# Kernel optimization log

Hardware: AMD Instinct MI355X
Metric: run time of the kernel (lower is better)

## Reference

```python
import jax, jax.numpy as jnp
import numpy as np

B, T, IN, H, L, OUT = 32, 512, 256, 1024, 2, 256


def setup_inputs() -> dict:
    key = jax.random.key(0)
    ks = jax.random.split(key, 12)
    s_in = 1.0 / np.sqrt(H)
    inp = {
        "input": jax.random.normal(ks[0], (B, T, IN), dtype=jnp.float32),
        # layer 0 GRU params (PyTorch layout: [3H, in], gate order r,z,n)
        "w_ih0": jax.random.uniform(ks[1], (3 * H, IN), jnp.float32, -s_in, s_in),
        "w_hh0": jax.random.uniform(ks[2], (3 * H, H), jnp.float32, -s_in, s_in),
        "b_ih0": jax.random.uniform(ks[3], (3 * H,), jnp.float32, -s_in, s_in),
        "b_hh0": jax.random.uniform(ks[4], (3 * H,), jnp.float32, -s_in, s_in),
        # layer 1 GRU params
        "w_ih1": jax.random.uniform(ks[5], (3 * H, H), jnp.float32, -s_in, s_in),
        "w_hh1": jax.random.uniform(ks[6], (3 * H, H), jnp.float32, -s_in, s_in),
        "b_ih1": jax.random.uniform(ks[7], (3 * H,), jnp.float32, -s_in, s_in),
        "b_hh1": jax.random.uniform(ks[8], (3 * H,), jnp.float32, -s_in, s_in),
        # final linear
        "fc_w": jax.random.uniform(ks[9], (OUT, H), jnp.float32, -s_in, s_in),
        "fc_b": jax.random.uniform(ks[10], (OUT,), jnp.float32, -s_in, s_in),
    }
    return inp


def _gru_layer(x, h0, w_ih, w_hh, b_ih, b_hh):
    # x: [B, T, D]; h0: [B, H]. Precompute all input projections at once.
    gx = jnp.einsum("btd,gd->btg", x, w_ih) + b_ih  # [B, T, 3H]

    def step(h, gx_t):
        gh = h @ w_hh.T + b_hh  # [B, 3H]
        xr, xz, xn = jnp.split(gx_t, 3, axis=-1)
        hr, hz, hn = jnp.split(gh, 3, axis=-1)
        r = jax.nn.sigmoid(xr + hr)
        z = jax.nn.sigmoid(xz + hz)
        n = jnp.tanh(xn + r * hn)
        h_new = (1.0 - z) * n + z * h
        return h_new, h_new

    h_last, hs = jax.lax.scan(step, h0, jnp.swapaxes(gx, 0, 1))  # hs: [T, B, H]
    return jnp.swapaxes(hs, 0, 1), h_last


def reference(input, w_ih0, w_hh0, b_ih0, b_hh0, w_ih1, w_hh1, b_ih1, b_hh1, fc_w, fc_b):
    b = input.shape[0]
    h0 = jnp.zeros((b, H), dtype=input.dtype)
    out0, h_last0 = _gru_layer(input, h0, w_ih0, w_hh0, b_ih0, b_hh0)
    out1, h_last1 = _gru_layer(out0, h0, w_ih1, w_hh1, b_ih1, b_hh1)
    h_n = jnp.stack([h_last0, h_last1], axis=0)  # [L, B, H]
    logits = out1[:, -1, :] @ fc_w.T + fc_b  # [B, OUT]
    return jax.nn.sigmoid(logits), h_n
```

## Files before the change

kernel.cpp:

```cpp
#include <hip/hip_runtime.h>

#define BB 32
#define TT 512
#define INW 256
#define HH 1024
#define OUTW 256
#define SLOT 32768

typedef __attribute__((ext_vector_type(8))) short short8;
typedef __attribute__((ext_vector_type(4))) float floatx4;
typedef __attribute__((ext_vector_type(4))) unsigned int uint4v;

#define SENT 0x7F807F80u

#define RSWZ(i) ((i) ^ ((((i) >> 5) & 3) << 2))

__device__ __forceinline__ unsigned short f2bf(float f) {
    unsigned int u = __float_as_uint(f);
    u = (u + 0x7fffu + ((u >> 16) & 1u)) >> 16;
    return (unsigned short)u;
}
__device__ __forceinline__ float bf2f(unsigned short h) {
    return __uint_as_float(((unsigned int)h) << 16);
}
__device__ __forceinline__ float fast_tanh(float x) {
    return 2.f / (1.f + __expf(-2.f * x)) - 1.f;
}
__device__ __forceinline__ float tree8(const float* p) {
    return ((p[0] + p[1]) + (p[2] + p[3])) + ((p[4] + p[5]) + (p[6] + p[7]));
}

__global__ void cast_f32_bf16(const float* __restrict__ src,
                              unsigned short* __restrict__ dst, int n) {
    int i = blockIdx.x * blockDim.x + threadIdx.x;
    int stride = gridDim.x * blockDim.x;
    for (; i < n; i += stride) dst[i] = f2bf(src[i]);
}

__global__ void fill_sent(uint4v* __restrict__ dst, size_t n4) {
    size_t i = (size_t)blockIdx.x * blockDim.x + threadIdx.x;
    size_t stride = (size_t)gridDim.x * blockDim.x;
    uint4v v = {SENT, SENT, SENT, SENT};
    for (; i < n4; i += stride) dst[i] = v;
}

template <int K>
__global__ __launch_bounds__(256) void gemm_gx(const unsigned short* __restrict__ X,
                                               const unsigned short* __restrict__ W,
                                               const float* __restrict__ bias,
                                               unsigned short* __restrict__ Cout) {
    __shared__ __align__(16) unsigned short As[64 * 40];
    __shared__ __align__(16) unsigned short Bs[64 * 40];
    int bid = blockIdx.x;
    int tn = bid % 48, tm = bid / 48;
    int tid = threadIdx.x;
    int lane = tid & 63, wv = tid >> 6;
    int wm = wv >> 1, wn = wv & 1;
    int l15 = lane & 15, q = lane >> 4;
    floatx4 acc[2][2] = {};
    int r = tid >> 2, kq = (tid & 3) * 8;
    const unsigned short* xrow = X + (size_t)(tm * 64 + r) * K;
    const unsigned short* wrow = W + (size_t)(tn * 64 + r) * K;
    const int NK = K / 32;
    for (int kk = 0; kk < NK; ++kk) {
        int k0 = kk * 32;
        *(short8*)&As[r * 40 + kq] = *(const short8*)&xrow[k0 + kq];
        *(short8*)&Bs[r * 40 + kq] = *(const short8*)&wrow[k0 + kq];
        __syncthreads();
        short8 a0 = *(const short8*)&As[(wm * 32 + l15) * 40 + q * 8];
        short8 a1 = *(const short8*)&As[(wm * 32 + 16 + l15) * 40 + q * 8];
        short8 b0 = *(const short8*)&Bs[(wn * 32 + l15) * 40 + q * 8];
        short8 b1 = *(const short8*)&Bs[(wn * 32 + 16 + l15) * 40 + q * 8];
        acc[0][0] = __builtin_amdgcn_mfma_f32_16x16x32_bf16(a0, b0, acc[0][0], 0, 0, 0);
        acc[0][1] = __builtin_amdgcn_mfma_f32_16x16x32_bf16(a0, b1, acc[0][1], 0, 0, 0);
        acc[1][0] = __builtin_amdgcn_mfma_f32_16x16x32_bf16(a1, b0, acc[1][0], 0, 0, 0);
        acc[1][1] = __builtin_amdgcn_mfma_f32_16x16x32_bf16(a1, b1, acc[1][1], 0, 0, 0);
        __syncthreads();
    }
    for (int mi = 0; mi < 2; ++mi)
        for (int ni = 0; ni < 2; ++ni) {
            int col = tn * 64 + wn * 32 + ni * 16 + l15;
            float bv = bias[col];
            int row0 = tm * 64 + wm * 32 + mi * 16 + q * 4;
            for (int rr = 0; rr < 4; ++rr) {
                Cout[(size_t)(row0 + rr) * 3072 + col] = f2bf(acc[mi][ni][rr] + bv);
            }
        }
}

__global__ __launch_bounds__(512, 2) void gru_fused(
    const unsigned short* __restrict__ gx0, const unsigned short* __restrict__ whh0,
    const float* __restrict__ bhh0, const unsigned short* __restrict__ wih1,
    const unsigned short* __restrict__ whh1, const float* __restrict__ bih1,
    const float* __restrict__ bhh1, unsigned short* __restrict__ ring0,
    unsigned short* __restrict__ ring1, float* __restrict__ hn0,
    float* __restrict__ hn1, unsigned int* __restrict__ flags) {
    __shared__ __align__(16) float red[8 * 6 * 64 * 4];
    const int bid = blockIdx.x;
    const int tid = threadIdx.x;
    const int lane = tid & 63, wv = tid >> 6;
    const int l15 = lane & 15, q = lane >> 4;
    const int gb = tid >> 3, gjh = tid & 7;
    const int gmi = gb >> 4, greg = gb & 3;
    const int grl = ((gb & 15) >> 2) * 16 + 2 * gjh;

    if (bid < 64) {
        const int j0 = bid * 16;
        const int kbase = wv * 128;
        const unsigned int* fl0 = flags + ((bid & 7) << 8);
        short8 Wr[4], Wz[4], Wn[4];
        {
            const unsigned short* wr0 = whh0 + (size_t)(j0 + l15) * HH;
            const unsigned short* wr1 = whh0 + (size_t)(1024 + j0 + l15) * HH;
            const unsigned short* wr2 = whh0 + (size_t)(2048 + j0 + l15) * HH;
#pragma unroll
            for (int s = 0; s < 4; ++s) {
                int k = kbase + s * 32 + q * 8;
                Wr[s] = *(const short8*)&wr0[k];
                Wz[s] = *(const short8*)&wr1[k];
                Wn[s] = *(const short8*)&wr2[k];
            }
        }
        float bR[2], bZ[2], bN[2], hpriv[2] = {0.f, 0.f};
        unsigned int pxr = 0, pxz = 0, pxn = 0;
        const unsigned short* gxp = nullptr;
        if (tid < 256) {
            int jj = j0 + 2 * gjh;
#pragma unroll
            for (int i = 0; i < 2; ++i) {
                bR[i] = bhh0[jj + i];
                bZ[i] = bhh0[1024 + jj + i];
                bN[i] = bhh0[2048 + jj + i];
            }
            gxp = gx0 + (size_t)gb * TT * 3072 + jj;
            pxr = *(const unsigned int*)(gxp);
            pxz = *(const unsigned int*)(gxp + 1024);
            pxn = *(const unsigned int*)(gxp + 2048);
        }

        for (int t = 0; t < TT; ++t) {
            if (t > 0 && wv == 0) {
                unsigned int target = (unsigned int)t;
                while (true) {
                    unsigned int v = __hip_atomic_load(fl0 + lane, __ATOMIC_RELAXED,
                                                       __HIP_MEMORY_SCOPE_AGENT);
                    if (__all((int)(v >= target))) break;
                }
            }
            __syncthreads();
            const unsigned short* hc = ring0 + (size_t)t * SLOT;
            unsigned int cxr = pxr, cxz = pxz, cxn = pxn;

            const unsigned short* ap[4];
#pragma unroll
            for (int s = 0; s < 4; ++s) {
                int k = kbase + s * 32 + q * 8;
                ap[s] = hc + ((k >> 4) << 9) + (l15 << 4) + (k & 15);
            }
            uint4v r0[4], r1[4];
            while (true) {
#pragma unroll
                for (int s = 0; s < 4; ++s) {
                    asm volatile("global_load_dwordx4 %0, %1, off sc0 sc1"
                                 : "=&v"(r0[s]) : "v"(ap[s]));
                    asm volatile("global_load_dwordx4 %0, %1, off offset:512 sc0 sc1"
                                 : "=&v"(r1[s]) : "v"(ap[s]));
                }
                asm volatile("s_waitcnt vmcnt(0)"
                             : "+v"(r0[0]), "+v"(r0[1]), "+v"(r0[2]), "+v"(r0[3]),
                               "+v"(r1[0]), "+v"(r1[1]), "+v"(r1[2]), "+v"(r1[3])
                             :: "memory");
                unsigned bad = 0;
#pragma unroll
                for (int s = 0; s < 4; ++s) {
                    bad |= (unsigned)(r0[s][0] == SENT) | (unsigned)(r0[s][1] == SENT) |
                           (unsigned)(r0[s][2] == SENT) | (unsigned)(r0[s][3] == SENT);
                    bad |= (unsigned)(r1[s][0] == SENT) | (unsigned)(r1[s][1] == SENT) |
                           (unsigned)(r1[s][2] == SENT) | (unsigned)(r1[s][3] == SENT);
                }
                if (!__any((int)bad)) break;
            }

            floatx4 acc[6] = {};
#pragma unroll
            for (int s = 0; s < 4; ++s) {
                short8 a0 = __builtin_bit_cast(short8, r0[s]);
                short8 a1 = __builtin_bit_cast(short8, r1[s]);
                acc[0] = __builtin_amdgcn_mfma_f32_16x16x32_bf16(a0, Wr[s], acc[0], 0, 0, 0);
                acc[1] = __builtin_amdgcn_mfma_f32_16x16x32_bf16(a0, Wz[s], acc[1], 0, 0, 0);
                acc[2] = __builtin_amdgcn_mfma_f32_16x16x32_bf16(a0, Wn[s], acc[2], 0, 0, 0);
                acc[3] = __builtin_amdgcn_mfma_f32_16x16x32_bf16(a1, Wr[s], acc[3], 0, 0, 0);
                acc[4] = __builtin_amdgcn_mfma_f32_16x16x32_bf16(a1, Wz[s], acc[4], 0, 0, 0);
                acc[5] = __builtin_amdgcn_mfma_f32_16x16x32_bf16(a1, Wn[s], acc[5], 0, 0, 0);
            }
#pragma unroll
            for (int tl = 0; tl < 6; ++tl)
                *(floatx4*)&red[RSWZ(((wv * 6 + tl) * 64 + lane) * 4)] = acc[tl];
            __syncthreads();

            float hnew[2];
            if (tid < 256) {
#pragma unroll
                for (int i = 0; i < 2; ++i) {
                    int rl = grl + i;
                    float pr[8], pz[8], pn[8];
#pragma unroll
                    for (int w = 0; w < 8; ++w) {
                        pr[w] = red[RSWZ(((w * 6 + gmi * 3 + 0) * 64 + rl) * 4 + greg)];
                        pz[w] = red[RSWZ(((w * 6 + gmi * 3 + 1) * 64 + rl) * 4 + greg)];
                        pn[w] = red[RSWZ(((w * 6 + gmi * 3 + 2) * 64 + rl) * 4 + greg)];
                    }
                    float gr = tree8(pr), gz = tree8(pz), gn = tree8(pn);
                    float xr = bf2f((unsigned short)(i ? (cxr >> 16) : (cxr & 0xffffu)));
                    float xz = bf2f((unsigned short)(i ? (cxz >> 16) : (cxz & 0xffffu)));
                    float xn = bf2f((unsigned short)(i ? (cxn >> 16) : (cxn & 0xffffu)));
                    float rg = 1.f / (1.f + __expf(-(xr + gr + bR[i])));
                    float zg = 1.f / (1.f + __expf(-(xz + gz + bZ[i])));
                    float ng = fast_tanh(xn + rg * (gn + bN[i]));
                    hnew[i] = (1.f - zg) * ng + zg * hpriv[i];
                    hpriv[i] = hnew[i];
                }
                unsigned int hpack =
                    (unsigned int)f2bf(hnew[0]) | ((unsigned int)f2bf(hnew[1]) << 16);
                unsigned int* dst =
                    (unsigned int*)(ring0 + (size_t)(t + 1) * SLOT) + (bid << 8) + tid;
                __hip_atomic_store(dst, hpack, __ATOMIC_RELAXED,
                                   __HIP_MEMORY_SCOPE_AGENT);
            }
            __syncthreads();
            if (tid < 8)
                __hip_atomic_store(flags + (tid << 8) + bid, (unsigned int)(t + 1),
                                   __ATOMIC_RELAXED, __HIP_MEMORY_SCOPE_AGENT);
            if (tid < 256) {
                if (t == TT - 1) {
                    hn0[gb * HH + j0 + 2 * gjh] = hnew[0];
                    hn0[gb * HH + j0 + 2 * gjh + 1] = hnew[1];
                }
                if (t + 1 < TT) {
                    const unsigned short* g2 = gxp + (size_t)(t + 1) * 3072;
                    pxr = *(const unsigned int*)(g2);
                    pxz = *(const unsigned int*)(g2 + 1024);
                    pxn = *(const unsigned int*)(g2 + 2048);
                }
            }
        }
    } else {
        const int b2 = bid - 64;
        const int j0 = b2 * 16;
        const bool isx = (wv >= 4);
        const int kbase = (wv & 3) * 256;
        const unsigned int* fl1 = flags + 2048 + ((b2 & 7) << 8);
        const unsigned int* fl0 = flags + ((b2 & 7) << 8);
        short8 Wr[8], Wz[8], Wn[8];
        {
            const unsigned short* wsrc = isx ? wih1 : whh1;
            const unsigned short* w0 = wsrc + (size_t)(j0 + l15) * HH;
            const unsigned short* w1 = wsrc + (size_t)(1024 + j0 + l15) * HH;
            const unsigned short* w2 = wsrc + (size_t)(2048 + j0 + l15) * HH;
#pragma unroll
            for (int s = 0; s < 8; ++s) {
                int k = kbase + s * 32 + q * 8;
                Wr[s] = *(const short8*)&w0[k];
                Wz[s] = *(const short8*)&w1[k];
                Wn[s] = *(const short8*)&w2[k];
            }
        }
        float cR[2], cZ[2], cNx[2], cNh[2], hpriv[2] = {0.f, 0.f};
        if (tid < 256) {
            int jj = j0 + 2 * gjh;
#pragma unroll
            for (int i = 0; i < 2; ++i) {
                cR[i] = bih1[jj + i] + bhh1[jj + i];
                cZ[i] = bih1[1024 + jj + i] + bhh1[1024 + jj + i];
                cNx[i] = bih1[2048 + jj + i];
                cNh[i] = bhh1[2048 + jj + i];
            }
        }

        for (int t = 0; t < TT; ++t) {
            if (t > 0 && wv == 0) {
                unsigned int target = (unsigned int)t;
                while (true) {
                    unsigned int v = __hip_atomic_load(fl1 + lane, __ATOMIC_RELAXED,
                                                       __HIP_MEMORY_SCOPE_AGENT);
                    if (__all((int)(v >= target))) break;
                }
            }
            if (wv == 4) {
                unsigned int target = (unsigned int)(t + 1);
                while (true) {
                    unsigned int v = __hip_atomic_load(fl0 + lane, __ATOMIC_RELAXED,
                                                       __HIP_MEMORY_SCOPE_AGENT);
                    if (__all((int)(v >= target))) break;
                }
            }
            __syncthreads();
            const unsigned short* src =
                isx ? (ring0 + (size_t)(t + 1) * SLOT) : (ring1 + (size_t)t * SLOT);

            const unsigned short* ap[8];
#pragma unroll
            for (int s = 0; s < 8; ++s) {
                int k = kbase + s * 32 + q * 8;
                ap[s] = src + ((k >> 4) << 9) + (l15 << 4) + (k & 15);
            }
            uint4v r0[8], r1[8];
            while (true) {
#pragma unroll
                for (int s = 0; s < 8; ++s) {
                    asm volatile("global_load_dwordx4 %0, %1, off sc0 sc1"
                                 : "=&v"(r0[s]) : "v"(ap[s]));
                    asm volatile("global_load_dwordx4 %0, %1, off offset:512 sc0 sc1"
                                 : "=&v"(r1[s]) : "v"(ap[s]));
                }
                asm volatile("s_waitcnt vmcnt(0)"
                             : "+v"(r0[0]), "+v"(r0[1]), "+v"(r0[2]), "+v"(r0[3]),
                               "+v"(r0[4]), "+v"(r0[5]), "+v"(r0[6]), "+v"(r0[7]),
                               "+v"(r1[0]), "+v"(r1[1]), "+v"(r1[2]), "+v"(r1[3]),
                               "+v"(r1[4]), "+v"(r1[5]), "+v"(r1[6]), "+v"(r1[7])
                             :: "memory");
                unsigned bad = 0;
#pragma unroll
                for (int s = 0; s < 8; ++s) {
                    bad |= (unsigned)(r0[s][0] == SENT) | (unsigned)(r0[s][1] == SENT) |
                           (unsigned)(r0[s][2] == SENT) | (unsigned)(r0[s][3] == SENT);
                    bad |= (unsigned)(r1[s][0] == SENT) | (unsigned)(r1[s][1] == SENT) |
                           (unsigned)(r1[s][2] == SENT) | (unsigned)(r1[s][3] == SENT);
                }
                if (!__any((int)bad)) break;
            }

            floatx4 acc[6] = {};
#pragma unroll
            for (int s = 0; s < 8; ++s) {
                short8 a0 = __builtin_bit_cast(short8, r0[s]);
                short8 a1 = __builtin_bit_cast(short8, r1[s]);
                acc[0] = __builtin_amdgcn_mfma_f32_16x16x32_bf16(a0, Wr[s], acc[0], 0, 0, 0);
                acc[1] = __builtin_amdgcn_mfma_f32_16x16x32_bf16(a0, Wz[s], acc[1], 0, 0, 0);
                acc[2] = __builtin_amdgcn_mfma_f32_16x16x32_bf16(a0, Wn[s], acc[2], 0, 0, 0);
                acc[3] = __builtin_amdgcn_mfma_f32_16x16x32_bf16(a1, Wr[s], acc[3], 0, 0, 0);
                acc[4] = __builtin_amdgcn_mfma_f32_16x16x32_bf16(a1, Wz[s], acc[4], 0, 0, 0);
                acc[5] = __builtin_amdgcn_mfma_f32_16x16x32_bf16(a1, Wn[s], acc[5], 0, 0, 0);
            }
#pragma unroll
            for (int tl = 0; tl < 6; ++tl)
                *(floatx4*)&red[RSWZ(((wv * 6 + tl) * 64 + lane) * 4)] = acc[tl];
            __syncthreads();

            float hnew[2];
            if (tid < 256) {
#pragma unroll
                for (int i = 0; i < 2; ++i) {
                    int rl = grl + i;
                    float pr[8], pz[8], ph[4], px[4];
#pragma unroll
                    for (int w = 0; w < 8; ++w) {
                        pr[w] = red[RSWZ(((w * 6 + gmi * 3 + 0) * 64 + rl) * 4 + greg)];
                        pz[w] = red[RSWZ(((w * 6 + gmi * 3 + 1) * 64 + rl) * 4 + greg)];
                    }
#pragma unroll
                    for (int w = 0; w < 4; ++w)
                        ph[w] = red[RSWZ(((w * 6 + gmi * 3 + 2) * 64 + rl) * 4 + greg)];
#pragma unroll
                    for (int w = 4; w < 8; ++w)
                        px[w - 4] = red[RSWZ(((w * 6 + gmi * 3 + 2) * 64 + rl) * 4 + greg)];
                    float gr = tree8(pr), gz = tree8(pz);
                    float hn = (ph[0] + ph[1]) + (ph[2] + ph[3]);
                    float xn = (px[0] + px[1]) + (px[2] + px[3]);
                    float rg = 1.f / (1.f + __expf(-(gr + cR[i])));
                    float zg = 1.f / (1.f + __expf(-(gz + cZ[i])));
                    float ng = fast_tanh(xn + cNx[i] + rg * (hn + cNh[i]));
                    hnew[i] = (1.f - zg) * ng + zg * hpriv[i];
                    hpriv[i] = hnew[i];
                }
                unsigned int hpack =
                    (unsigned int)f2bf(hnew[0]) | ((unsigned int)f2bf(hnew[1]) << 16);
                unsigned int* dst =
                    (unsigned int*)(ring1 + (size_t)(t + 1) * SLOT) + (b2 << 8) + tid;
                __hip_atomic_store(dst, hpack, __ATOMIC_RELAXED,
                                   __HIP_MEMORY_SCOPE_AGENT);
            }
            __syncthreads();
            if (tid < 8)
                __hip_atomic_store(flags + 2048 + (tid << 8) + b2, (unsigned int)(t + 1),
                                   __ATOMIC_RELAXED, __HIP_MEMORY_SCOPE_AGENT);
            if (tid < 256 && t == TT - 1) {
                hn1[gb * HH + j0 + 2 * gjh] = hnew[0];
                hn1[gb * HH + j0 + 2 * gjh + 1] = hnew[1];
            }
        }
    }
}

__global__ void fc_out(const unsigned short* __restrict__ h1bf,
                       const float* __restrict__ fcw, const float* __restrict__ fcb,
                       float* __restrict__ out) {
    int b = blockIdx.x, o = threadIdx.x;
    const float* wr = fcw + (size_t)o * HH;
    float acc = fcb[o];
    for (int k = 0; k < HH; k += 16) {
        const unsigned short* hp = h1bf + ((k >> 4) << 9) + (b << 4);
#pragma unroll
        for (int i = 0; i < 16; ++i) acc += bf2f(hp[i]) * wr[k + i];
    }
    out[b * OUTW + o] = 1.f / (1.f + expf(-acc));
}

extern "C" void kernel_launch(void* const* d_in, const int* in_sizes, int n_in,
                              void* d_out, int out_size, void* d_ws, size_t ws_size,
                              hipStream_t stream) {
    (void)in_sizes; (void)n_in; (void)out_size; (void)ws_size;
    const float* input = (const float*)d_in[0];
    const float* w_ih0 = (const float*)d_in[1];
    const float* w_hh0 = (const float*)d_in[2];
    const float* b_ih0 = (const float*)d_in[3];
    const float* b_hh0 = (const float*)d_in[4];
    const float* w_ih1 = (const float*)d_in[5];
    const float* w_hh1 = (const float*)d_in[6];
    const float* b_ih1 = (const float*)d_in[7];
    const float* b_hh1 = (const float*)d_in[8];
    const float* fc_w = (const float*)d_in[9];
    const float* fc_b = (const float*)d_in[10];
    float* out = (float*)d_out;

    char* ws = (char*)d_ws;
    size_t off = 0;
    auto alloc = [&](size_t bytes) {
        void* p = ws + off;
        off += (bytes + 255) & ~(size_t)255;
        return p;
    };
    unsigned int* flags = (unsigned int*)alloc(16384);
    unsigned short* ring0 = (unsigned short*)alloc((size_t)(TT + 1) * SLOT * 2);
    unsigned short* ring1 = (unsigned short*)alloc((size_t)(TT + 1) * SLOT * 2);
    unsigned short* gx0 = (unsigned short*)alloc((size_t)16384 * 3072 * 2);
    unsigned short* in_bf = (unsigned short*)alloc((size_t)16384 * 256 * 2);
    unsigned short* wih0_bf = (unsigned short*)alloc((size_t)3072 * 256 * 2);
    unsigned short* whh0_bf = (unsigned short*)alloc((size_t)3072 * 1024 * 2);
    unsigned short* wih1_bf = (unsigned short*)alloc((size_t)3072 * 1024 * 2);
    unsigned short* whh1_bf = (unsigned short*)alloc((size_t)3072 * 1024 * 2);

    {
        size_t total_bytes = (size_t)2 * (TT + 1) * SLOT * 2;
        fill_sent<<<1024, 256, 0, stream>>>((uint4v*)ring0, total_bytes / 16);
    }

    cast_f32_bf16<<<256, 256, 0, stream>>>(input, in_bf, 16384 * 256);
    cast_f32_bf16<<<64, 256, 0, stream>>>(w_ih0, wih0_bf, 3072 * 256);
    cast_f32_bf16<<<256, 256, 0, stream>>>(w_hh0, whh0_bf, 3072 * 1024);
    cast_f32_bf16<<<256, 256, 0, stream>>>(w_ih1, wih1_bf, 3072 * 1024);
    cast_f32_bf16<<<256, 256, 0, stream>>>(w_hh1, whh1_bf, 3072 * 1024);

    hipMemsetAsync(flags, 0, 16384, stream);
    hipMemsetAsync(ring0, 0, (size_t)SLOT * 2, stream);
    hipMemsetAsync(ring1, 0, (size_t)SLOT * 2, stream);

    gemm_gx<256><<<12288, 256, 0, stream>>>(in_bf, wih0_bf, b_ih0, gx0);

    gru_fused<<<128, 512, 0, stream>>>(gx0, whh0_bf, b_hh0, wih1_bf, whh1_bf, b_ih1,
                                       b_hh1, ring0, ring1, out + 8192,
                                       out + 8192 + 32768, flags);

    fc_out<<<32, 256, 0, stream>>>(ring1 + (size_t)TT * SLOT, fc_w, fc_b, out);
}
```

Baseline: 2.455 ms.

## Drop flag barriers, rely on sentinel polling and split matmul/gate warps

Removes the per-step flag arrays and atomic flag polling, so consumers detect readiness only by spinning on sentinel values in the ring buffers. Layer 0 now uses four matmul warps over K=256 each and four dedicated gate warps, and the gate step for t-1 runs concurrently with the matmul for t, software-pipelining the recurrence. Layer 1 gate warps likewise compute the previous step's output before issuing their input-projection loads. This is meant to cut cross-block synchronisation latency per timestep, at the cost of heavier register use per warp (the occupancy hint is dropped) and reliance on sentinel-only visibility ordering.

```diff
diff --git a/kernel.cpp b/kernel.cpp
--- a/kernel.cpp
+++ b/kernel.cpp
@@ -88,43 +88,100 @@
         }
 }
 
-__global__ __launch_bounds__(512, 2) void gru_fused(
+__device__ __forceinline__ void spin_load8(const unsigned short* base, int kbase,
+                                           int l15, int q, uint4v r0[8],
+                                           uint4v r1[8]) {
+    const unsigned short* ap[8];
+#pragma unroll
+    for (int s = 0; s < 8; ++s) {
+        int k = kbase + s * 32 + q * 8;
+        ap[s] = base + ((k >> 4) << 9) + (l15 << 4) + (k & 15);
+    }
+    while (true) {
+#pragma unroll
+        for (int s = 0; s < 8; ++s) {
+            asm volatile("global_load_dwordx4 %0, %1, off sc0 sc1"
+                         : "=&v"(r0[s]) : "v"(ap[s]));
+            asm volatile("global_load_dwordx4 %0, %1, off offset:512 sc0 sc1"
+                         : "=&v"(r1[s]) : "v"(ap[s]));
+        }
+        asm volatile("s_waitcnt vmcnt(0)"
+                     : "+v"(r0[0]), "+v"(r0[1]), "+v"(r0[2]), "+v"(r0[3]),
+                       "+v"(r0[4]), "+v"(r0[5]), "+v"(r0[6]), "+v"(r0[7]),
+                       "+v"(r1[0]), "+v"(r1[1]), "+v"(r1[2]), "+v"(r1[3]),
+                       "+v"(r1[4]), "+v"(r1[5]), "+v"(r1[6]), "+v"(r1[7])
+                     :: "memory");
+        unsigned bad = 0;
+#pragma unroll
+        for (int s = 0; s < 8; ++s) {
+            bad |= (unsigned)(r0[s][0] == SENT) | (unsigned)(r0[s][1] == SENT) |
+                   (unsigned)(r0[s][2] == SENT) | (unsigned)(r0[s][3] == SENT);
+            bad |= (unsigned)(r1[s][0] == SENT) | (unsigned)(r1[s][1] == SENT) |
+                   (unsigned)(r1[s][2] == SENT) | (unsigned)(r1[s][3] == SENT);
+        }
+        if (!__any((int)bad)) break;
+    }
+}
+
+__device__ __forceinline__ void mfma8(const uint4v r0[8], const uint4v r1[8],
+                                      const short8 Wr[8], const short8 Wz[8],
+                                      const short8 Wn[8], floatx4 acc[6]) {
+#pragma unroll
+    for (int s = 0; s < 8; ++s) {
+        short8 a0 = __builtin_bit_cast(short8, r0[s]);
+        short8 a1 = __builtin_bit_cast(short8, r1[s]);
+        acc[0] = __builtin_amdgcn_mfma_f32_16x16x32_bf16(a0, Wr[s], acc[0], 0, 0, 0);
+        acc[1] = __builtin_amdgcn_mfma_f32_16x16x32_bf16(a0, Wz[s], acc[1], 0, 0, 0);
+        acc[2] = __builtin_amdgcn_mfma_f32_16x16x32_bf16(a0, Wn[s], acc[2], 0, 0, 0);
+        acc[3] = __builtin_amdgcn_mfma_f32_16x16x32_bf16(a1, Wr[s], acc[3], 0, 0, 0);
+        acc[4] = __builtin_amdgcn_mfma_f32_16x16x32_bf16(a1, Wz[s], acc[4], 0, 0, 0);
+        acc[5] = __builtin_amdgcn_mfma_f32_16x16x32_bf16(a1, Wn[s], acc[5], 0, 0, 0);
+    }
+}
+
+__device__ __forceinline__ void hoist_w(const unsigned short* wsrc, int j0, int l15,
+                                        int q, int kbase, short8 Wr[8], short8 Wz[8],
+                                        short8 Wn[8]) {
+    const unsigned short* w0 = wsrc + (size_t)(j0 + l15) * HH;
+    const unsigned short* w1 = wsrc + (size_t)(1024 + j0 + l15) * HH;
+    const unsigned short* w2 = wsrc + (size_t)(2048 + j0 + l15) * HH;
+#pragma unroll
+    for (int s = 0; s < 8; ++s) {
+        int k = kbase + s * 32 + q * 8;
+        Wr[s] = *(const short8*)&w0[k];
+        Wz[s] = *(const short8*)&w1[k];
+        Wn[s] = *(const short8*)&w2[k];
+    }
+}
+
+__global__ __launch_bounds__(512) void gru_fused(
     const unsigned short* __restrict__ gx0, const unsigned short* __restrict__ whh0,
     const float* __restrict__ bhh0, const unsigned short* __restrict__ wih1,
     const unsigned short* __restrict__ whh1, const float* __restrict__ bih1,
     const float* __restrict__ bhh1, unsigned short* __restrict__ ring0,
     unsigned short* __restrict__ ring1, float* __restrict__ hn0,
-    float* __restrict__ hn1, unsigned int* __restrict__ flags) {
+    float* __restrict__ hn1) {
     __shared__ __align__(16) float red[8 * 6 * 64 * 4];
     const int bid = blockIdx.x;
     const int tid = threadIdx.x;
     const int lane = tid & 63, wv = tid >> 6;
     const int l15 = lane & 15, q = lane >> 4;
-    const int gb = tid >> 3, gjh = tid & 7;
+    const bool isGate = (wv >= 4);
+    const int gtid = tid & 255;
+    const int gb = gtid >> 3, gjh = gtid & 7;
     const int gmi = gb >> 4, greg = gb & 3;
     const int grl = ((gb & 15) >> 2) * 16 + 2 * gjh;
 
     if (bid < 64) {
         const int j0 = bid * 16;
-        const int kbase = wv * 128;
-        const unsigned int* fl0 = flags + ((bid & 7) << 8);
-        short8 Wr[4], Wz[4], Wn[4];
-        {
-            const unsigned short* wr0 = whh0 + (size_t)(j0 + l15) * HH;
-            const unsigned short* wr1 = whh0 + (size_t)(1024 + j0 + l15) * HH;
-            const unsigned short* wr2 = whh0 + (size_t)(2048 + j0 + l15) * HH;
-#pragma unroll
-            for (int s = 0; s < 4; ++s) {
-                int k = kbase + s * 32 + q * 8;
-                Wr[s] = *(const short8*)&wr0[k];
-                Wz[s] = *(const short8*)&wr1[k];
-                Wn[s] = *(const short8*)&wr2[k];
-            }
-        }
+        const int kbase = (wv & 3) * 256;
+        short8 Wr[8], Wz[8], Wn[8];
+        if (!isGate) hoist_w(whh0, j0, l15, q, kbase, Wr, Wz, Wn);
+
         float bR[2], bZ[2], bN[2], hpriv[2] = {0.f, 0.f};
         unsigned int pxr = 0, pxz = 0, pxn = 0;
         const unsigned short* gxp = nullptr;
-        if (tid < 256) {
+        if (isGate) {
             int jj = j0 + 2 * gjh;
 #pragma unroll
             for (int i = 0; i < 2; ++i) {
@@ -138,79 +195,38 @@
             pxn = *(const unsigned int*)(gxp + 2048);
         }
 
-        for (int t = 0; t < TT; ++t) {
-            if (t > 0 && wv == 0) {
-                unsigned int target = (unsigned int)t;
-                while (true) {
-                    unsigned int v = __hip_atomic_load(fl0 + lane, __ATOMIC_RELAXED,
-                                                       __HIP_MEMORY_SCOPE_AGENT);
-                    if (__all((int)(v >= target))) break;
-                }
-            }
-            __syncthreads();
-            const unsigned short* hc = ring0 + (size_t)t * SLOT;
-            unsigned int cxr = pxr, cxz = pxz, cxn = pxn;
-
-            const unsigned short* ap[4];
-#pragma unroll
-            for (int s = 0; s < 4; ++s) {
-                int k = kbase + s * 32 + q * 8;
-                ap[s] = hc + ((k >> 4) << 9) + (l15 << 4) + (k & 15);
-            }
-            uint4v r0[4], r1[4];
-            while (true) {
-#pragma unroll
-                for (int s = 0; s < 4; ++s) {
-                    asm volatile("global_load_dwordx4 %0, %1, off sc0 sc1"
-                                 : "=&v"(r0[s]) : "v"(ap[s]));
-                    asm volatile("global_load_dwordx4 %0, %1, off offset:512 sc0 sc1"
-                                 : "=&v"(r1[s]) : "v"(ap[s]));
-                }
-                asm volatile("s_waitcnt vmcnt(0)"
-                             : "+v"(r0[0]), "+v"(r0[1]), "+v"(r0[2]), "+v"(r0[3]),
-                               "+v"(r1[0]), "+v"(r1[1]), "+v"(r1[2]), "+v"(r1[3])
-                             :: "memory");
-                unsigned bad = 0;
-#pragma unroll
-                for (int s = 0; s < 4; ++s) {
-                    bad |= (unsigned)(r0[s][0] == SENT) | (unsigned)(r0[s][1] == SENT) |
-                           (unsigned)(r0[s][2] == SENT) | (unsigned)(r0[s][3] == SENT);
-                    bad |= (unsigned)(r1[s][0] == SENT) | (unsigned)(r1[s][1] == SENT) |
-                           (unsigned)(r1[s][2] == SENT) | (unsigned)(r1[s][3] == SENT);
-                }
-                if (!__any((int)bad)) break;
-            }
-
+        for (int t = 0; t <= TT; ++t) {
             floatx4 acc[6] = {};
-#pragma unroll
-            for (int s = 0; s < 4; ++s) {
-                short8 a0 = __builtin_bit_cast(short8, r0[s]);
-                short8 a1 = __builtin_bit_cast(short8, r1[s]);
-                acc[0] = __builtin_amdgcn_mfma_f32_16x16x32_bf16(a0, Wr[s], acc[0], 0, 0, 0);
-                acc[1] = __builtin_amdgcn_mfma_f32_16x16x32_bf16(a0, Wz[s], acc[1], 0, 0, 0);
-                acc[2] = __builtin_amdgcn_mfma_f32_16x16x32_bf16(a0, Wn[s], acc[2], 0, 0, 0);
-                acc[3] = __builtin_amdgcn_mfma_f32_16x16x32_bf16(a1, Wr[s], acc[3], 0, 0, 0);
-                acc[4] = __builtin_amdgcn_mfma_f32_16x16x32_bf16(a1, Wz[s], acc[4], 0, 0, 0);
-                acc[5] = __builtin_amdgcn_mfma_f32_16x16x32_bf16(a1, Wn[s], acc[5], 0, 0, 0);
-            }
-#pragma unroll
-            for (int tl = 0; tl < 6; ++tl)
-                *(floatx4*)&red[RSWZ(((wv * 6 + tl) * 64 + lane) * 4)] = acc[tl];
-            __syncthreads();
-
-            float hnew[2];
-            if (tid < 256) {
+            bool doW = false;
+            if (!isGate) {
+                if (t < TT) {
+                    uint4v r0[8], r1[8];
+                    spin_load8(ring0 + (size_t)t * SLOT, kbase, l15, q, r0, r1);
+                    mfma8(r0, r1, Wr, Wz, Wn, acc);
+                    doW = true;
+                }
+            } else if (t > 0) {
+                unsigned int cxr = pxr, cxz = pxz, cxn = pxn;
+                if (t < TT) {
+                    const unsigned short* g2 = gxp + (size_t)t * 3072;
+                    pxr = *(const unsigned int*)(g2);
+                    pxz = *(const unsigned int*)(g2 + 1024);
+                    pxn = *(const unsigned int*)(g2 + 2048);
+                }
+                float hnew[2];
 #pragma unroll
                 for (int i = 0; i < 2; ++i) {
                     int rl = grl + i;
-                    float pr[8], pz[8], pn[8];
-#pragma unroll
-                    for (int w = 0; w < 8; ++w) {
+                    float pr[4], pz[4], pn[4];
+#pragma unroll
+                    for (int w = 0; w < 4; ++w) {
                         pr[w] = red[RSWZ(((w * 6 + gmi * 3 + 0) * 64 + rl) * 4 + greg)];
                         pz[w] = red[RSWZ(((w * 6 + gmi * 3 + 1) * 64 + rl) * 4 + greg)];
                         pn[w] = red[RSWZ(((w * 6 + gmi * 3 + 2) * 64 + rl) * 4 + greg)];
                     }
-                    float gr = tree8(pr), gz = tree8(pz), gn = tree8(pn);
+                    float gr = (pr[0] + pr[1]) + (pr[2] + pr[3]);
+                    float gz = (pz[0] + pz[1]) + (pz[2] + pz[3]);
+                    float gn = (pn[0] + pn[1]) + (pn[2] + pn[3]);
                     float xr = bf2f((unsigned short)(i ? (cxr >> 16) : (cxr & 0xffffu)));
                     float xz = bf2f((unsigned short)(i ? (cxz >> 16) : (cxz & 0xffffu)));
                     float xn = bf2f((unsigned short)(i ? (cxn >> 16) : (cxn & 0xffffu)));
@@ -223,50 +239,31 @@
                 unsigned int hpack =
                     (unsigned int)f2bf(hnew[0]) | ((unsigned int)f2bf(hnew[1]) << 16);
                 unsigned int* dst =
-                    (unsigned int*)(ring0 + (size_t)(t + 1) * SLOT) + (bid << 8) + tid;
+                    (unsigned int*)(ring0 + (size_t)t * SLOT) + (bid << 8) + gtid;
                 __hip_atomic_store(dst, hpack, __ATOMIC_RELAXED,
                                    __HIP_MEMORY_SCOPE_AGENT);
-            }
-            __syncthreads();
-            if (tid < 8)
-                __hip_atomic_store(flags + (tid << 8) + bid, (unsigned int)(t + 1),
-                                   __ATOMIC_RELAXED, __HIP_MEMORY_SCOPE_AGENT);
-            if (tid < 256) {
-                if (t == TT - 1) {
+                if (t == TT) {
                     hn0[gb * HH + j0 + 2 * gjh] = hnew[0];
                     hn0[gb * HH + j0 + 2 * gjh + 1] = hnew[1];
                 }
-                if (t + 1 < TT) {
-                    const unsigned short* g2 = gxp + (size_t)(t + 1) * 3072;
-                    pxr = *(const unsigned int*)(g2);
-                    pxz = *(const unsigned int*)(g2 + 1024);
-                    pxn = *(const unsigned int*)(g2 + 2048);
-                }
-            }
+            }
+            __syncthreads();
+            if (doW) {
+#pragma unroll
+                for (int tl = 0; tl < 6; ++tl)
+                    *(floatx4*)&red[RSWZ((((wv & 3) * 6 + tl) * 64 + lane) * 4)] = acc[tl];
+            }
+            __syncthreads();
         }
     } else {
         const int b2 = bid - 64;
         const int j0 = b2 * 16;
-        const bool isx = (wv >= 4);
         const int kbase = (wv & 3) * 256;
-        const unsigned int* fl1 = flags + 2048 + ((b2 & 7) << 8);
-        const unsigned int* fl0 = flags + ((b2 & 7) << 8);
         short8 Wr[8], Wz[8], Wn[8];
-        {
-            const unsigned short* wsrc = isx ? wih1 : whh1;
-            const unsigned short* w0 = wsrc + (size_t)(j0 + l15) * HH;
-            const unsigned short* w1 = wsrc + (size_t)(1024 + j0 + l15) * HH;
-            const unsigned short* w2 = wsrc + (size_t)(2048 + j0 + l15) * HH;
-#pragma unroll
-            for (int s = 0; s < 8; ++s) {
-                int k = kbase + s * 32 + q * 8;
-                Wr[s] = *(const short8*)&w0[k];
-                Wz[s] = *(const short8*)&w1[k];
-                Wn[s] = *(const short8*)&w2[k];
-            }
-        }
+        hoist_w(isGate ? wih1 : whh1, j0, l15, q, kbase, Wr, Wz, Wn);
+
         float cR[2], cZ[2], cNx[2], cNh[2], hpriv[2] = {0.f, 0.f};
-        if (tid < 256) {
+        if (isGate) {
             int jj = j0 + 2 * gjh;
 #pragma unroll
             for (int i = 0; i < 2; ++i) {
@@ -277,117 +274,68 @@
             }
         }
 
-        for (int t = 0; t < TT; ++t) {
-            if (t > 0 && wv == 0) {
-                unsigned int target = (unsigned int)t;
-                while (true) {
-                    unsigned int v = __hip_atomic_load(fl1 + lane, __ATOMIC_RELAXED,
-                                                       __HIP_MEMORY_SCOPE_AGENT);
-                    if (__all((int)(v >= target))) break;
-                }
-            }
-            if (wv == 4) {
-                unsigned int target = (unsigned int)(t + 1);
-                while (true) {
-                    unsigned int v = __hip_atomic_load(fl0 + lane, __ATOMIC_RELAXED,
-                                                       __HIP_MEMORY_SCOPE_AGENT);
-                    if (__all((int)(v >= target))) break;
+        for (int t = 0; t <= TT; ++t) {
+            floatx4 acc[6] = {};
+            bool doW = false;
+            if (!isGate) {
+                if (t < TT) {
+                    uint4v r0[8], r1[8];
+                    spin_load8(ring1 + (size_t)t * SLOT, kbase, l15, q, r0, r1);
+                    mfma8(r0, r1, Wr, Wz, Wn, acc);
+                    doW = true;
+                }
+            } else {
+                if (t > 0) {
+                    float hnew[2];
+#pragma unroll
+                    for (int i = 0; i < 2; ++i) {
+                        int rl = grl + i;
+                        float pr[8], pz[8], ph[4], px[4];
+#pragma unroll
+                        for (int w = 0; w < 8; ++w) {
+                            pr[w] = red[RSWZ(((w * 6 + gmi * 3 + 0) * 64 + rl) * 4 + greg)];
+                            pz[w] = red[RSWZ(((w * 6 + gmi * 3 + 1) * 64 + rl) * 4 + greg)];
+                        }
+#pragma unroll
+                        for (int w = 0; w < 4; ++w)
+                            ph[w] = red[RSWZ(((w * 6 + gmi * 3 + 2) * 64 + rl) * 4 + greg)];
+#pragma unroll
+                        for (int w = 4; w < 8; ++w)
+                            px[w - 4] = red[RSWZ(((w * 6 + gmi * 3 + 2) * 64 + rl) * 4 + greg)];
+                        float gr = tree8(pr), gz = tree8(pz);
+                        float hn = (ph[0] + ph[1]) + (ph[2] + ph[3]);
+                        float xn = (px[0] + px[1]) + (px[2] + px[3]);
+                        float rg = 1.f / (1.f + __expf(-(gr + cR[i])));
+                        float zg = 1.f / (1.f + __expf(-(gz + cZ[i])));
+                        float ng = fast_tanh(xn + cNx[i] + rg * (hn + cNh[i]));
+                        hnew[i] = (1.f - zg) * ng + zg * hpriv[i];
+                        hpriv[i] = hnew[i];
+                    }
+                    unsigned int hpack =
+                        (unsigned int)f2bf(hnew[0]) | ((unsigned int)f2bf(hnew[1]) << 16);
+                    unsigned int* dst =
+                        (unsigned int*)(ring1 + (size_t)t * SLOT) + (b2 << 8) + gtid;
+                    __hip_atomic_store(dst, hpack, __ATOMIC_RELAXED,
+                                       __HIP_MEMORY_SCOPE_AGENT);
+                    if (t == TT) {
+                        hn1[gb * HH + j0 + 2 * gjh] = hnew[0];
+                        hn1[gb * HH + j0 + 2 * gjh + 1] = hnew[1];
+                    }
+                }
+                if (t < TT) {
+                    uint4v r0[8], r1[8];
+                    spin_load8(ring0 + (size_t)(t + 1) * SLOT, kbase, l15, q, r0, r1);
+                    mfma8(r0, r1, Wr, Wz, Wn, acc);
+                    doW = true;
                 }
             }
             __syncthreads();
-            const unsigned short* src =
-                isx ? (ring0 + (size_t)(t + 1) * SLOT) : (ring1 + (size_t)t * SLOT);
-
-            const unsigned short* ap[8];
-#pragma unroll
-            for (int s = 0; s < 8; ++s) {
-                int k = kbase + s * 32 + q * 8;
-                ap[s] = src + ((k >> 4) << 9) + (l15 << 4) + (k & 15);
-            }
-            uint4v r0[8], r1[8];
-            while (true) {
-#pragma unroll
-                for (int s = 0; s < 8; ++s) {
-                    asm volatile("global_load_dwordx4 %0, %1, off sc0 sc1"
-                                 : "=&v"(r0[s]) : "v"(ap[s]));
-                    asm volatile("global_load_dwordx4 %0, %1, off offset:512 sc0 sc1"
-                                 : "=&v"(r1[s]) : "v"(ap[s]));
-                }
-                asm volatile("s_waitcnt vmcnt(0)"
-                             : "+v"(r0[0]), "+v"(r0[1]), "+v"(r0[2]), "+v"(r0[3]),
-                               "+v"(r0[4]), "+v"(r0[5]), "+v"(r0[6]), "+v"(r0[7]),
-                               "+v"(r1[0]), "+v"(r1[1]), "+v"(r1[2]), "+v"(r1[3]),
-                               "+v"(r1[4]), "+v"(r1[5]), "+v"(r1[6]), "+v"(r1[7])
-                             :: "memory");
-                unsigned bad = 0;
-#pragma unroll
-                for (int s = 0; s < 8; ++s) {
-                    bad |= (unsigned)(r0[s][0] == SENT) | (unsigned)(r0[s][1] == SENT) |
-                           (unsigned)(r0[s][2] == SENT) | (unsigned)(r0[s][3] == SENT);
-                    bad |= (unsigned)(r1[s][0] == SENT) | (unsigned)(r1[s][1] == SENT) |
-                           (unsigned)(r1[s][2] == SENT) | (unsigned)(r1[s][3] == SENT);
-                }
-                if (!__any((int)bad)) break;
-            }
-
-            floatx4 acc[6] = {};
-#pragma unroll
-            for (int s = 0; s < 8; ++s) {
-                short8 a0 = __builtin_bit_cast(short8, r0[s]);
-                short8 a1 = __builtin_bit_cast(short8, r1[s]);
-                acc[0] = __builtin_amdgcn_mfma_f32_16x16x32_bf16(a0, Wr[s], acc[0], 0, 0, 0);
-                acc[1] = __builtin_amdgcn_mfma_f32_16x16x32_bf16(a0, Wz[s], acc[1], 0, 0, 0);
-                acc[2] = __builtin_amdgcn_mfma_f32_16x16x32_bf16(a0, Wn[s], acc[2], 0, 0, 0);
-                acc[3] = __builtin_amdgcn_mfma_f32_16x16x32_bf16(a1, Wr[s], acc[3], 0, 0, 0);
-                acc[4] = __builtin_amdgcn_mfma_f32_16x16x32_bf16(a1, Wz[s], acc[4], 0, 0, 0);
-                acc[5] = __builtin_amdgcn_mfma_f32_16x16x32_bf16(a1, Wn[s], acc[5], 0, 0, 0);
-            }
-#pragma unroll
-            for (int tl = 0; tl < 6; ++tl)
-                *(floatx4*)&red[RSWZ(((wv * 6 + tl) * 64 + lane) * 4)] = acc[tl];
+            if (doW) {
+#pragma unroll
+                for (int tl = 0; tl < 6; ++tl)
+                    *(floatx4*)&red[RSWZ(((wv * 6 + tl) * 64 + lane) * 4)] = acc[tl];
+            }
             __syncthreads();
-
-            float hnew[2];
-            if (tid < 256) {
-#pragma unroll
-                for (int i = 0; i < 2; ++i) {
-                    int rl = grl + i;
-                    float pr[8], pz[8], ph[4], px[4];
-#pragma unroll
-                    for (int w = 0; w < 8; ++w) {
-                        pr[w] = red[RSWZ(((w * 6 + gmi * 3 + 0) * 64 + rl) * 4 + greg)];
-                        pz[w] = red[RSWZ(((w * 6 + gmi * 3 + 1) * 64 + rl) * 4 + greg)];
-                    }
-#pragma unroll
-                    for (int w = 0; w < 4; ++w)
-                        ph[w] = red[RSWZ(((w * 6 + gmi * 3 + 2) * 64 + rl) * 4 + greg)];
-#pragma unroll
-                    for (int w = 4; w < 8; ++w)
-                        px[w - 4] = red[RSWZ(((w * 6 + gmi * 3 + 2) * 64 + rl) * 4 + greg)];
-                    float gr = tree8(pr), gz = tree8(pz);
-                    float hn = (ph[0] + ph[1]) + (ph[2] + ph[3]);
-                    float xn = (px[0] + px[1]) + (px[2] + px[3]);
-                    float rg = 1.f / (1.f + __expf(-(gr + cR[i])));
-                    float zg = 1.f / (1.f + __expf(-(gz + cZ[i])));
-                    float ng = fast_tanh(xn + cNx[i] + rg * (hn + cNh[i]));
-                    hnew[i] = (1.f - zg) * ng + zg * hpriv[i];
-                    hpriv[i] = hnew[i];
-                }
-                unsigned int hpack =
-                    (unsigned int)f2bf(hnew[0]) | ((unsigned int)f2bf(hnew[1]) << 16);
-                unsigned int* dst =
-                    (unsigned int*)(ring1 + (size_t)(t + 1) * SLOT) + (b2 << 8) + tid;
-                __hip_atomic_store(dst, hpack, __ATOMIC_RELAXED,
-                                   __HIP_MEMORY_SCOPE_AGENT);
-            }
-            __syncthreads();
-            if (tid < 8)
-                __hip_atomic_store(flags + 2048 + (tid << 8) + b2, (unsigned int)(t + 1),
-                                   __ATOMIC_RELAXED, __HIP_MEMORY_SCOPE_AGENT);
-            if (tid < 256 && t == TT - 1) {
-                hn1[gb * HH + j0 + 2 * gjh] = hnew[0];
-                hn1[gb * HH + j0 + 2 * gjh + 1] = hnew[1];
-            }
         }
     }
 }
@@ -430,7 +378,6 @@
         off += (bytes + 255) & ~(size_t)255;
         return p;
     };
-    unsigned int* flags = (unsigned int*)alloc(16384);
     unsigned short* ring0 = (unsigned short*)alloc((size_t)(TT + 1) * SLOT * 2);
     unsigned short* ring1 = (unsigned short*)alloc((size_t)(TT + 1) * SLOT * 2);
     unsigned short* gx0 = (unsigned short*)alloc((size_t)16384 * 3072 * 2);
@@ -451,7 +398,6 @@
     cast_f32_bf16<<<256, 256, 0, stream>>>(w_ih1, wih1_bf, 3072 * 1024);
     cast_f32_bf16<<<256, 256, 0, stream>>>(w_hh1, whh1_bf, 3072 * 1024);
 
-    hipMemsetAsync(flags, 0, 16384, stream);
     hipMemsetAsync(ring0, 0, (size_t)SLOT * 2, stream);
     hipMemsetAsync(ring1, 0, (size_t)SLOT * 2, stream);
 
@@ -459,7 +405,7 @@
 
     gru_fused<<<128, 512, 0, stream>>>(gx0, whh0_bf, b_hh0, wih1_bf, whh1_bf, b_ih1,
                                        b_hh1, ring0, ring1, out + 8192,
-                                       out + 8192 + 32768, flags);
+                                       out + 8192 + 32768);
 
     fc_out<<<32, 256, 0, stream>>>(ring1 + (size_t)TT * SLOT, fc_w, fc_b, out);
 }
```

Result: faster. 2.200 ms (-10.4%).
